# Kernel optimization log

Hardware: AMD Instinct MI355X
Metric: run time of the kernel (lower is better)

Reference implementation:

```python
import jax, jax.numpy as jnp
import numpy as np

D_MODEL = 192
D_STATE = 16
D_CONV = 4
EXPAND = 2
D_INNER = EXPAND * D_MODEL          # 384
DT_RANK = (D_MODEL + 15) // 16       # 12
B_, C_, DD, HH, WW = 2, 192, 32, 32, 16


def setup_inputs() -> dict:
    key = jax.random.key(0)
    ks = jax.random.split(key, 10)
    s = 0.02
    return {
        "x": jax.random.normal(ks[0], (B_, C_, DD, HH, WW), jnp.float32),
        # Mamba params (mamba-ssm layout)
        "in_proj_w": jax.random.normal(ks[1], (2 * D_INNER, D_MODEL), jnp.float32) * s,
        "conv_w": jax.random.normal(ks[2], (D_INNER, 1, D_CONV), jnp.float32) * s,
        "conv_b": jnp.zeros((D_INNER,), jnp.float32),
        "x_proj_w": jax.random.normal(ks[3], (DT_RANK + 2 * D_STATE, D_INNER), jnp.float32) * s,
        "dt_proj_w": jax.random.normal(ks[4], (D_INNER, DT_RANK), jnp.float32) * s,
        # bias chosen so softplus(dt) is small/positive, as in mamba's dt init
        "dt_proj_b": jax.random.uniform(ks[5], (D_INNER,), jnp.float32, minval=-4.0, maxval=-2.0),
        "A_log": jnp.log(jnp.broadcast_to(jnp.arange(1, D_STATE + 1, dtype=jnp.float32), (D_INNER, D_STATE))),
        "D_param": jnp.ones((D_INNER,), jnp.float32),
        "out_proj_w": jax.random.normal(ks[6], (D_MODEL, D_INNER), jnp.float32) * s,
        # 1x1x1 Conv3d projection (input_dim -> output_dim)
        "proj_w": jax.random.normal(ks[7], (C_, C_), jnp.float32) * s,
        "proj_b": jnp.zeros((C_,), jnp.float32),
    }


def _mamba(xf, in_proj_w, conv_w, conv_b, x_proj_w, dt_proj_w, dt_proj_b, A_log, D_param, out_proj_w):
    # xf: (B, L, d_model)
    B, L, _ = xf.shape
    xz = xf @ in_proj_w.T                          # (B, L, 2*d_inner)
    u, z = jnp.split(xz, 2, axis=-1)               # each (B, L, d_inner)

    # causal depthwise conv1d over L, kernel D_CONV
    uc = jnp.transpose(u, (0, 2, 1))               # (B, d_inner, L)
    up = jnp.pad(uc, ((0, 0), (0, 0), (D_CONV - 1, 0)))
    conv = sum(up[:, :, k:k + L] * conv_w[None, :, 0, k, None] for k in range(D_CONV))
    conv = conv + conv_b[None, :, None]
    u = jax.nn.silu(jnp.transpose(conv, (0, 2, 1)))  # (B, L, d_inner)

    dbl = u @ x_proj_w.T                           # (B, L, dt_rank + 2*d_state)
    dt_low = dbl[..., :DT_RANK]
    Bm = dbl[..., DT_RANK:DT_RANK + D_STATE]       # (B, L, d_state)
    Cm = dbl[..., DT_RANK + D_STATE:]              # (B, L, d_state)
    dt = jax.nn.softplus(dt_low @ dt_proj_w.T + dt_proj_b)  # (B, L, d_inner)

    A = -jnp.exp(A_log)                            # (d_inner, d_state)

    def step(h, inputs):
        u_t, dt_t, B_t, C_t = inputs               # (B,d_inner),(B,d_inner),(B,d_state),(B,d_state)
        dA = jnp.exp(dt_t[..., None] * A)          # (B, d_inner, d_state)
        h = dA * h + dt_t[..., None] * B_t[:, None, :] * u_t[..., None]
        y = jnp.einsum('bds,bs->bd', h, C_t)
        return h, y

    h0 = jnp.zeros((B, D_INNER, D_STATE), xf.dtype)
    xs = (jnp.transpose(u, (1, 0, 2)), jnp.transpose(dt, (1, 0, 2)),
          jnp.transpose(Bm, (1, 0, 2)), jnp.transpose(Cm, (1, 0, 2)))
    _, ys = jax.lax.scan(step, h0, xs)             # ys: (L, B, d_inner)
    y = jnp.transpose(ys, (1, 0, 2)) + u * D_param
    y = y * jax.nn.silu(z)
    return y @ out_proj_w.T                        # (B, L, d_model)


def reference(x, in_proj_w, conv_w, conv_b, x_proj_w, dt_proj_w, dt_proj_b,
              A_log, D_param, out_proj_w, proj_w, proj_b):
    B, C, Dz, H, W = x.shape
    # InstanceNorm3d (affine=False, eps=1e-5, biased variance)
    mu = x.mean(axis=(2, 3, 4), keepdims=True)
    var = x.var(axis=(2, 3, 4), keepdims=True)
    xn = (x - mu) / jnp.sqrt(var + 1e-5)
    L = Dz * H * W
    xf = jnp.transpose(xn.reshape(B, C, L), (0, 2, 1))  # (B, L, C)
    y = _mamba(xf, in_proj_w, conv_w, conv_b, x_proj_w, dt_proj_w, dt_proj_b,
               A_log, D_param, out_proj_w)
    y = jnp.transpose(y, (0, 2, 1)).reshape(B, C, Dz, H, W)
    # 1x1x1 Conv3d projection
    out = jnp.einsum('bcdhw,oc->bodhw', y, proj_w) + proj_b[None, :, None, None, None]
    return out
```

## Files before the change

kernel.cpp:

```cpp
#include <hip/hip_runtime.h>
#include <hip/hip_bf16.h>
#include <hip/hip_fp16.h>
#include <math.h>

#define BB   2
#define CM   192
#define DI   384
#define LL   16384
#define NST  16
#define RDT  12
#define XJ   44
#define NC   512
#define CLEN 32
#define NCH  (NC / 16)
#define DBS  64
#define XZS  768
#define CVT  32
#define BK   32

typedef __attribute__((ext_vector_type(8))) short bf16x8;
typedef __attribute__((ext_vector_type(4))) float f32x4;
typedef __attribute__((ext_vector_type(2))) float f32x2;
typedef unsigned short ushort_t;

static __device__ __forceinline__ ushort_t f2bf(float f) {
  __hip_bfloat16 h = __float2bfloat16(f);
  return *reinterpret_cast<ushort_t*>(&h);
}
static __device__ __forceinline__ float bf2f(ushort_t u) {
  __hip_bfloat16 h;
  *reinterpret_cast<ushort_t*>(&h) = u;
  return __bfloat162float(h);
}
static __device__ __forceinline__ ushort_t f2h(float f) {
  __half h = __float2half(f);
  return *reinterpret_cast<ushort_t*>(&h);
}
static __device__ __forceinline__ float h2f(ushort_t u) {
  __half h;
  *reinterpret_cast<ushort_t*>(&h) = u;
  return __half2float(h);
}
static __device__ __forceinline__ unsigned pk2bf(float lo, float hi) {
  return (unsigned)f2bf(lo) | ((unsigned)f2bf(hi) << 16);
}

__global__ __launch_bounds__(256) void fuse_proj_kernel(
    const float* __restrict__ pw, const float* __restrict__ ow, float* __restrict__ PW) {
  int idx = blockIdx.x * 256 + threadIdx.x;
  if (idx >= CM * DI) return;
  int o = idx / DI, d = idx % DI;
  float s = 0.f;
  #pragma unroll 4
  for (int c = 0; c < CM; c++) s += pw[o * CM + c] * ow[c * DI + d];
  PW[idx] = s;
}

__global__ __launch_bounds__(256) void cvt_weights_kernel(
    const float* __restrict__ ipw, const float* __restrict__ xpw,
    const float* __restrict__ PW,
    ushort_t* __restrict__ ipw_bf, ushort_t* __restrict__ xpw_bf,
    ushort_t* __restrict__ PW_bf) {
  int i = blockIdx.x * 256 + threadIdx.x;
  if (i < 2 * DI * CM) ipw_bf[i] = f2bf(ipw[i]);
  if (i < 128 * DI) {
    int r = i / DI;
    xpw_bf[i] = (r < XJ) ? f2bf(xpw[i]) : (ushort_t)0;
  }
  if (i < 256 * DI) {
    int r = i / DI;
    PW_bf[i] = (r < CM) ? f2bf(PW[i]) : (ushort_t)0;
  }
}

__global__ __launch_bounds__(256) void norm_stats_kernel(
    const float* __restrict__ x, float* __restrict__ mu, float* __restrict__ rstd) {
  int bc = blockIdx.x;
  const float* p = x + (size_t)bc * LL;
  float s = 0.f, ss = 0.f;
  for (int i = threadIdx.x * 4; i < LL; i += 256 * 4) {
    float4 v = *(const float4*)(p + i);
    s += v.x + v.y + v.z + v.w;
    ss += v.x * v.x + v.y * v.y + v.z * v.z + v.w * v.w;
  }
  for (int o = 32; o > 0; o >>= 1) {
    s += __shfl_down(s, o, 64);
    ss += __shfl_down(ss, o, 64);
  }
  __shared__ float sb[4], ssb[4];
  int wid = threadIdx.x >> 6;
  if ((threadIdx.x & 63) == 0) { sb[wid] = s; ssb[wid] = ss; }
  __syncthreads();
  if (threadIdx.x == 0) {
    s = sb[0] + sb[1] + sb[2] + sb[3];
    ss = ssb[0] + ssb[1] + ssb[2] + ssb[3];
    float m = s * (1.f / LL);
    float var = ss * (1.f / LL) - m * m;
    mu[bc] = m;
    rstd[bc] = 1.f / sqrtf(var + 1e-5f);
  }
}

__global__ __launch_bounds__(256) void xt_norm_kernel(
    const float* __restrict__ x, const float* __restrict__ mu,
    const float* __restrict__ rstd, ushort_t* __restrict__ xT) {
  __shared__ ushort_t T[64][72];
  int t0 = blockIdx.x * 64, c0 = blockIdx.y * 64, b = blockIdx.z;
  int tid = threadIdx.x;
  int c = tid >> 2, tq = (tid & 3) * 16;
  int bc = b * CM + c0 + c;
  const float* xp = x + (size_t)bc * LL + t0 + tq;
  float m = mu[bc], rs = rstd[bc];
  #pragma unroll
  for (int j = 0; j < 16; j += 4) {
    float4 v = *(const float4*)(xp + j);
    T[c][tq + j + 0] = f2bf((v.x - m) * rs);
    T[c][tq + j + 1] = f2bf((v.y - m) * rs);
    T[c][tq + j + 2] = f2bf((v.z - m) * rs);
    T[c][tq + j + 3] = f2bf((v.w - m) * rs);
  }
  __syncthreads();
  int t = tid >> 2, cq = (tid & 3) * 16;
  unsigned int ob[8];
  #pragma unroll
  for (int j = 0; j < 8; j++)
    ob[j] = (unsigned int)T[cq + 2 * j][t] | ((unsigned int)T[cq + 2 * j + 1][t] << 16);
  ushort_t* op = xT + ((size_t)b * LL + t0 + t) * CM + c0 + cq;
  *(uint4*)(op)     = make_uint4(ob[0], ob[1], ob[2], ob[3]);
  *(uint4*)(op + 8) = make_uint4(ob[4], ob[5], ob[6], ob[7]);
}

template <bool TOUT, typename OutT>
__global__ __launch_bounds__(256) void gemm_lds(
    const ushort_t* __restrict__ A, const ushort_t* __restrict__ BT,
    OutT* __restrict__ C, int K, int Mreal, int MT,
    long strideBT, long strideC, int ldc,
    const float* __restrict__ bias) {
  __shared__ ushort_t Asm[2][128 * BK];
  __shared__ ushort_t Bsm[2][128 * BK];

  int id = blockIdx.x;
  int per = MT * 8;
  int g = id / per, r = id % per;
  int nt = g * 8 + (r & 7);
  int mt = r >> 3;
  int b  = nt >> 7;
  long n0 = (long)(nt & 127) * 128;
  int m0 = mt * 128;

  int tid = threadIdx.x;
  int lane = tid & 63, wave = tid >> 6;
  const ushort_t* Bbase = BT + (size_t)b * strideBT;

  int srow0 = wave * 32 + (lane >> 2);
  int sk = (lane & 3) * 8;

  f32x4 acc[4][4];
  #pragma unroll
  for (int mi = 0; mi < 4; mi++)
    #pragma unroll
    for (int ni = 0; ni < 4; ni++) acc[mi][ni] = (f32x4){0.f, 0.f, 0.f, 0.f};

  int mh = wave & 1, nh = wave >> 1;
  int fr = lane & 15, fk = (lane >> 4) * 8;

  int nsteps = K / BK;
  {
    const ushort_t* As0 = A + (size_t)(m0 + srow0) * K + sk;
    const ushort_t* Bs0 = Bbase + (size_t)(n0 + srow0) * K + sk;
    __builtin_amdgcn_global_load_lds(As0, &Asm[0][wave * 1024], 16, 0, 0);
    __builtin_amdgcn_global_load_lds(As0 + (size_t)16 * K, &Asm[0][wave * 1024 + 512], 16, 0, 0);
    __builtin_amdgcn_global_load_lds(Bs0, &Bsm[0][wave * 1024], 16, 0, 0);
    __builtin_amdgcn_global_load_lds(Bs0 + (size_t)16 * K, &Bsm[0][wave * 1024 + 512], 16, 0, 0);
  }
  __syncthreads();
  int cur = 0;
  for (int s = 0; s < nsteps; s++) {
    if (s + 1 < nsteps) {
      int k0 = (s + 1) * BK;
      const ushort_t* As0 = A + (size_t)(m0 + srow0) * K + k0 + sk;
      const ushort_t* Bs0 = Bbase + (size_t)(n0 + srow0) * K + k0 + sk;
      __builtin_amdgcn_global_load_lds(As0, &Asm[cur ^ 1][wave * 1024], 16, 0, 0);
      __builtin_amdgcn_global_load_lds(As0 + (size_t)16 * K, &Asm[cur ^ 1][wave * 1024 + 512], 16, 0, 0);
      __builtin_amdgcn_global_load_lds(Bs0, &Bsm[cur ^ 1][wave * 1024], 16, 0, 0);
      __builtin_amdgcn_global_load_lds(Bs0 + (size_t)16 * K, &Bsm[cur ^ 1][wave * 1024 + 512], 16, 0, 0);
    }
    bf16x8 fa[4], fb[4];
    #pragma unroll
    for (int mi = 0; mi < 4; mi++)
      fa[mi] = *(const bf16x8*)&Asm[cur][(mh * 64 + mi * 16 + fr) * BK + fk];
    #pragma unroll
    for (int ni = 0; ni < 4; ni++)
      fb[ni] = *(const bf16x8*)&Bsm[cur][(nh * 64 + ni * 16 + fr) * BK + fk];
    #pragma unroll
    for (int mi = 0; mi < 4; mi++)
      #pragma unroll
      for (int ni = 0; ni < 4; ni++) {
        if constexpr (TOUT)
          acc[mi][ni] = __builtin_amdgcn_mfma_f32_16x16x32_bf16(fb[ni], fa[mi], acc[mi][ni], 0, 0, 0);
        else
          acc[mi][ni] = __builtin_amdgcn_mfma_f32_16x16x32_bf16(fa[mi], fb[ni], acc[mi][ni], 0, 0, 0);
      }
    __syncthreads();
    cur ^= 1;
  }

  int cq = (lane >> 4) * 4;
  if constexpr (TOUT) {
    #pragma unroll
    for (int ni = 0; ni < 4; ni++)
      #pragma unroll
      for (int rg = 0; rg < 4; rg++) {
        long n = n0 + nh * 64 + ni * 16 + cq + rg;
        OutT* cp = C + (size_t)b * strideC + n * ldc + m0 + mh * 64 + fr;
        #pragma unroll
        for (int mi = 0; mi < 4; mi++) {
          int mrow = m0 + mh * 64 + mi * 16 + fr;
          if (mrow < Mreal) {
            float v = acc[mi][ni][rg];
            if constexpr (sizeof(OutT) == 2) cp[mi * 16] = f2bf(v);
            else                             cp[mi * 16] = v;
          }
        }
      }
  } else {
    #pragma unroll
    for (int mi = 0; mi < 4; mi++)
      #pragma unroll
      for (int rg = 0; rg < 4; rg++) {
        int m = m0 + mh * 64 + mi * 16 + cq + rg;
        if (m < Mreal) {
          float bv = bias ? bias[m] : 0.f;
          OutT* cp = C + (size_t)b * strideC + (size_t)m * ldc + n0 + nh * 64 + fr;
          #pragma unroll
          for (int ni = 0; ni < 4; ni++)
            cp[ni * 16] = acc[mi][ni][rg] + bv;
        }
      }
  }
}

__global__ __launch_bounds__(384) void conv_silu_kernel(
    const ushort_t* __restrict__ xzT, const float* __restrict__ conv_w,
    const float* __restrict__ conv_b, ushort_t* __restrict__ u_t) {
  __shared__ ushort_t Us[CVT + 3][DI];
  int t0 = blockIdx.x * CVT;
  int b = blockIdx.y;
  int tid = threadIdx.x;
  #pragma unroll
  for (int r = 0; r < CVT + 3; r++) {
    int t = t0 - 3 + r;
    Us[r][tid] = (t >= 0) ? xzT[((size_t)b * LL + t) * XZS + tid] : (ushort_t)0;
  }
  float w0 = conv_w[tid * 4 + 0], w1 = conv_w[tid * 4 + 1];
  float w2 = conv_w[tid * 4 + 2], w3 = conv_w[tid * 4 + 3];
  float cb = conv_b[tid];
  __syncthreads();
  ushort_t* up = u_t + ((size_t)b * LL + t0) * DI + tid;
  float xm3 = bf2f(Us[0][tid]);
  float xm2 = bf2f(Us[1][tid]);
  float xm1 = bf2f(Us[2][tid]);
  #pragma unroll
  for (int t = 0; t < CVT; t++) {
    float xc = bf2f(Us[t + 3][tid]);
    float a = cb + w3 * xc + w2 * xm1 + w1 * xm2 + w0 * xm3;
    float sv = a / (1.f + __expf(-a));
    up[(size_t)t * DI] = f2bf(sv);
    xm3 = xm2; xm2 = xm1; xm1 = xc;
  }
}

__global__ __launch_bounds__(128) void scan_phase1(
    const ushort_t* __restrict__ u_t, const float* __restrict__ dblT,
    const float* __restrict__ A_log,
    const float* __restrict__ dtw, const float* __restrict__ dtb,
    ushort_t* __restrict__ hend, float* __restrict__ Sbuf,
    ushort_t* __restrict__ dt16) {
  int chunk = blockIdx.x, b = blockIdx.z;
  int d = blockIdx.y * 128 + threadIdx.x;
  int t0 = chunk * CLEN;
  const float* dblB = dblT + ((size_t)b * LL + t0) * DBS;
  int bd = b * DI + d;
  float av0 = -expf(A_log[d * NST]);
  float av_[NST];
  bool ok = true;
  #pragma unroll
  for (int j = 0; j < NST; j++) {
    av_[j] = -expf(A_log[d * NST + j]);
    ok = ok && (fabsf(av_[j] - av0 * (float)(j + 1)) <= 1e-4f * fabsf(av_[j]));
  }
  float w12[12];
  #pragma unroll
  for (int rr = 0; rr < 12; rr += 4)
    *(float4*)(w12 + rr) = *(const float4*)(dtw + d * 12 + rr);
  float db = dtb[d];
  const ushort_t* up = u_t + ((size_t)b * LL + t0) * DI + d;
  ushort_t* dtp16 = dt16 + ((size_t)b * LL + t0) * DI + d;
  float S = 0.f;

  size_t o = ((size_t)bd * NC + chunk) * NST;
  if (__all(ok)) {
    f32x2 h2[8];
    #pragma unroll
    for (int j = 0; j < 8; j++) h2[j] = (f32x2){0.f, 0.f};
    #pragma unroll 4
    for (int t = 0; t < CLEN; t++) {
      float4 L0 = *(const float4*)(dblB + t * DBS + 0);
      float4 L1 = *(const float4*)(dblB + t * DBS + 4);
      float4 L2 = *(const float4*)(dblB + t * DBS + 8);
      float4 B0 = *(const float4*)(dblB + t * DBS + RDT + 0);
      float4 B1 = *(const float4*)(dblB + t * DBS + RDT + 4);
      float4 B2 = *(const float4*)(dblB + t * DBS + RDT + 8);
      float4 B3 = *(const float4*)(dblB + t * DBS + RDT + 12);
      float acc = db;
      acc = fmaf(L0.x, w12[0], acc); acc = fmaf(L0.y, w12[1], acc);
      acc = fmaf(L0.z, w12[2], acc); acc = fmaf(L0.w, w12[3], acc);
      acc = fmaf(L1.x, w12[4], acc); acc = fmaf(L1.y, w12[5], acc);
      acc = fmaf(L1.z, w12[6], acc); acc = fmaf(L1.w, w12[7], acc);
      acc = fmaf(L2.x, w12[8], acc); acc = fmaf(L2.y, w12[9], acc);
      acc = fmaf(L2.z, w12[10], acc); acc = fmaf(L2.w, w12[11], acc);
      float dtv = (acc > 15.f) ? acc : __logf(1.f + __expf(acc));
      dtp16[(size_t)t * DI] = f2h(dtv);
      float uv  = bf2f(up[(size_t)t * DI]);
      float q = dtv * uv;
      S += dtv;
      float p1 = __expf(dtv * av0);
      float p2 = p1 * p1, p4 = p2 * p2, p8 = p4 * p4;
      f32x2 p2v = {p2, p2}, p4v = {p4, p4}, p8v = {p8, p8};
      f32x2 P0 = {p1, p2};
      f32x2 P1 = P0 * p2v;
      f32x2 P2 = P0 * p4v;
      f32x2 P3 = P1 * p4v;
      f32x2 P4 = P0 * p8v;
      f32x2 P5 = P1 * p8v;
      f32x2 P6 = P2 * p8v;
      f32x2 P7 = P3 * p8v;
      f32x2 qv = {q, q};
      h2[0] = P0 * h2[0] + qv * (f32x2){B0.x, B0.y};
      h2[1] = P1 * h2[1] + qv * (f32x2){B0.z, B0.w};
      h2[2] = P2 * h2[2] + qv * (f32x2){B1.x, B1.y};
      h2[3] = P3 * h2[3] + qv * (f32x2){B1.z, B1.w};
      h2[4] = P4 * h2[4] + qv * (f32x2){B2.x, B2.y};
      h2[5] = P5 * h2[5] + qv * (f32x2){B2.z, B2.w};
      h2[6] = P6 * h2[6] + qv * (f32x2){B3.x, B3.y};
      h2[7] = P7 * h2[7] + qv * (f32x2){B3.z, B3.w};
    }
    unsigned pk[8];
    #pragma unroll
    for (int j = 0; j < 8; j++) pk[j] = pk2bf(h2[j].x, h2[j].y);
    *(uint4*)(hend + o)     = make_uint4(pk[0], pk[1], pk[2], pk[3]);
    *(uint4*)(hend + o + 8) = make_uint4(pk[4], pk[5], pk[6], pk[7]);
  } else {
    float h[NST];
    #pragma unroll
    for (int j = 0; j < NST; j++) h[j] = 0.f;
    for (int t = 0; t < CLEN; t++) {
      float acc = db;
      #pragma unroll
      for (int rr = 0; rr < 12; rr++) acc = fmaf(dblB[t * DBS + rr], w12[rr], acc);
      float dtv = (acc > 15.f) ? acc : __logf(1.f + __expf(acc));
      dtp16[(size_t)t * DI] = f2h(dtv);
      float uv  = bf2f(up[(size_t)t * DI]);
      float q = dtv * uv;
      S += dtv;
      #pragma unroll
      for (int j = 0; j < NST; j++)
        h[j] = __expf(dtv * av_[j]) * h[j] + q * dblB[t * DBS + RDT + j];
    }
    #pragma unroll
    for (int j = 0; j < NST; j++) hend[o + j] = f2bf(h[j]);
  }
  Sbuf[(size_t)bd * NC + chunk] = S;
}

__global__ __launch_bounds__(256) void scan_combine(
    ushort_t* __restrict__ hend, const float* __restrict__ Sbuf,
    const float* __restrict__ A_log) {
  __shared__ float sP[16][16], sH[16][16];
  int bd = blockIdx.x;
  int d = bd % DI;
  int s = threadIdx.x & 15, g = threadIdx.x >> 4;
  float av = -expf(A_log[d * NST + s]);
  size_t baseS = (size_t)bd * NC + g * NCH;
  size_t base = ((size_t)bd * NC + g * NCH) * NST + s;
  float Pl = 1.f, Hl = 0.f;
  #pragma unroll
  for (int k = 0; k < NCH; k++) {
    float p = __expf(Sbuf[baseS + k] * av);
    Hl = fmaf(p, Hl, bf2f(hend[base + (size_t)k * NST]));
    Pl *= p;
  }
  sP[g][s] = Pl; sH[g][s] = Hl;
  __syncthreads();
  if (threadIdx.x < 16) {
    int ss = threadIdx.x;
    float c = 0.f;
    #pragma unroll
    for (int gg = 0; gg < 16; gg++) {
      float tmp = sH[gg][ss];
      float pp  = sP[gg][ss];
      sH[gg][ss] = c;
      c = fmaf(pp, c, tmp);
    }
  }
  __syncthreads();
  float c = sH[g][s];
  #pragma unroll
  for (int k = 0; k < NCH; k++) {
    size_t o = base + (size_t)k * NST;
    float p = __expf(Sbuf[baseS + k] * av);
    float he = bf2f(hend[o]);
    hend[o] = f2bf(c);
    c = fmaf(p, c, he);
  }
}

__global__ __launch_bounds__(128) void scan_phase3(
    const ushort_t* __restrict__ u_t, const float* __restrict__ dblT,
    const float* __restrict__ A_log, const ushort_t* __restrict__ dt16,
    const ushort_t* __restrict__ hin, const float* __restrict__ Dp,
    const ushort_t* __restrict__ xzT, ushort_t* __restrict__ ym_t) {
  int chunk = blockIdx.x, b = blockIdx.z;
  int d = blockIdx.y * 128 + threadIdx.x;
  int t0 = chunk * CLEN;
  const float* dblB = dblT + ((size_t)b * LL + t0) * DBS;
  int bd = b * DI + d;
  float av0 = -expf(A_log[d * NST]);
  float av_[NST];
  bool ok = true;
  #pragma unroll
  for (int j = 0; j < NST; j++) {
    av_[j] = -expf(A_log[d * NST + j]);
    ok = ok && (fabsf(av_[j] - av0 * (float)(j + 1)) <= 1e-4f * fabsf(av_[j]));
  }
  const ushort_t* up = u_t + ((size_t)b * LL + t0) * DI + d;
  const ushort_t* zp = xzT + ((size_t)b * LL + t0) * XZS + DI + d;
  const ushort_t* dtp16 = dt16 + ((size_t)b * LL + t0) * DI + d;
  ushort_t* ymp = ym_t + ((size_t)b * LL + t0) * DI + d;

  const ushort_t* hi = hin + ((size_t)bd * NC + chunk) * NST;
  float Dv = Dp[d];

  if (__all(ok)) {
    f32x2 h2[8];
    {
      uint4 q0 = *(const uint4*)(hi);
      uint4 q1 = *(const uint4*)(hi + 8);
      const unsigned* qw0 = (const unsigned*)&q0;
      const unsigned* qw1 = (const unsigned*)&q1;
      #pragma unroll
      for (int j = 0; j < 4; j++) {
        h2[j]     = (f32x2){bf2f((ushort_t)(qw0[j] & 0xffff)), bf2f((ushort_t)(qw0[j] >> 16))};
        h2[j + 4] = (f32x2){bf2f((ushort_t)(qw1[j] & 0xffff)), bf2f((ushort_t)(qw1[j] >> 16))};
      }
    }
    #pragma unroll 4
    for (int t = 0; t < CLEN; t++) {
      float4 B0 = *(const float4*)(dblB + t * DBS + RDT + 0);
      float4 B1 = *(const float4*)(dblB + t * DBS + RDT + 4);
      float4 B2 = *(const float4*)(dblB + t * DBS + RDT + 8);
      float4 B3 = *(const float4*)(dblB + t * DBS + RDT + 12);
      float4 C0 = *(const float4*)(dblB + t * DBS + RDT + 16);
      float4 C1 = *(const float4*)(dblB + t * DBS + RDT + 20);
      float4 C2 = *(const float4*)(dblB + t * DBS + RDT + 24);
      float4 C3 = *(const float4*)(dblB + t * DBS + RDT + 28);
      float dtv = h2f(dtp16[(size_t)t * DI]);
      float uv  = bf2f(up[(size_t)t * DI]);
      float zv  = bf2f(zp[(size_t)t * XZS]);
      float q = dtv * uv;
      float p1 = __expf(dtv * av0);
      float p2 = p1 * p1, p4 = p2 * p2, p8 = p4 * p4;
      f32x2 p2v = {p2, p2}, p4v = {p4, p4}, p8v = {p8, p8};
      f32x2 P0 = {p1, p2};
      f32x2 P1 = P0 * p2v;
      f32x2 P2 = P0 * p4v;
      f32x2 P3 = P1 * p4v;
      f32x2 P4 = P0 * p8v;
      f32x2 P5 = P1 * p8v;
      f32x2 P6 = P2 * p8v;
      f32x2 P7 = P3 * p8v;
      f32x2 qv = {q, q};
      f32x2 ya, yb;
      h2[0] = P0 * h2[0] + qv * (f32x2){B0.x, B0.y};  ya = h2[0] * (f32x2){C0.x, C0.y};
      h2[1] = P1 * h2[1] + qv * (f32x2){B0.z, B0.w};  yb = h2[1] * (f32x2){C0.z, C0.w};
      h2[2] = P2 * h2[2] + qv * (f32x2){B1.x, B1.y};  ya = h2[2] * (f32x2){C1.x, C1.y} + ya;
      h2[3] = P3 * h2[3] + qv * (f32x2){B1.z, B1.w};  yb = h2[3] * (f32x2){C1.z, C1.w} + yb;
      h2[4] = P4 * h2[4] + qv * (f32x2){B2.x, B2.y};  ya = h2[4] * (f32x2){C2.x, C2.y} + ya;
      h2[5] = P5 * h2[5] + qv * (f32x2){B2.z, B2.w};  yb = h2[5] * (f32x2){C2.z, C2.w} + yb;
      h2[6] = P6 * h2[6] + qv * (f32x2){B3.x, B3.y};  ya = h2[6] * (f32x2){C3.x, C3.y} + ya;
      h2[7] = P7 * h2[7] + qv * (f32x2){B3.z, B3.w};  yb = h2[7] * (f32x2){C3.z, C3.w} + yb;
      float y = (ya.x + ya.y) + (yb.x + yb.y);
      float yv = (y + uv * Dv) * (zv / (1.f + __expf(-zv)));
      ymp[(size_t)t * DI] = f2bf(yv);
    }
  } else {
    float h[NST];
    #pragma unroll
    for (int j = 0; j < NST; j++) h[j] = bf2f(hi[j]);
    for (int t = 0; t < CLEN; t++) {
      float dtv = h2f(dtp16[(size_t)t * DI]);
      float uv  = bf2f(up[(size_t)t * DI]);
      float zv  = bf2f(zp[(size_t)t * XZS]);
      float q = dtv * uv;
      float y = 0.f;
      #pragma unroll
      for (int j = 0; j < NST; j++) {
        h[j] = __expf(dtv * av_[j]) * h[j] + q * dblB[t * DBS + RDT + j];
        y = fmaf(h[j], dblB[t * DBS + RDT + NST + j], y);
      }
      float yv = (y + uv * Dv) * (zv / (1.f + __expf(-zv)));
      ymp[(size_t)t * DI] = f2bf(yv);
    }
  }
}

extern "C" void kernel_launch(void* const* d_in, const int* in_sizes, int n_in,
                              void* d_out, int out_size, void* d_ws, size_t ws_size,
                              hipStream_t stream) {
  const float* x         = (const float*)d_in[0];
  const float* in_proj_w = (const float*)d_in[1];
  const float* conv_w    = (const float*)d_in[2];
  const float* conv_b    = (const float*)d_in[3];
  const float* x_proj_w  = (const float*)d_in[4];
  const float* dt_proj_w = (const float*)d_in[5];
  const float* dt_proj_b = (const float*)d_in[6];
  const float* A_log     = (const float*)d_in[7];
  const float* D_param   = (const float*)d_in[8];
  const float* out_proj_w= (const float*)d_in[9];
  const float* proj_w    = (const float*)d_in[10];
  const float* proj_b    = (const float*)d_in[11];
  float* out = (float*)d_out;

  float* w = (float*)d_ws;
  float*    mu     = w;
  float*    rstd   = w + 512;
  float*    PW     = w + 1024;
  ushort_t* PW_bf  = (ushort_t*)(w + 74752);
  ushort_t* ipw_bf = (ushort_t*)(w + 123904);
  ushort_t* xpw_bf = (ushort_t*)(w + 197632);
  ushort_t* xT     = (ushort_t*)(w + 222208);
  ushort_t* xzT    = (ushort_t*)(w + 3367936);
  ushort_t* u_t    = (ushort_t*)(w + 15950848);
  float*    dblT   = w + 22242304;
  ushort_t* ym_t   = (ushort_t*)(w + 24339456);
  ushort_t* hend   = (ushort_t*)(w + 30630912);
  float*    Sbuf   = w + 33776640;
  ushort_t* dt16   = (ushort_t*)(w + 34169856);
  size_t need = 40461312;
  if (ws_size < need * sizeof(float)) return;

  norm_stats_kernel<<<dim3(BB * CM), dim3(256), 0, stream>>>(x, mu, rstd);
  fuse_proj_kernel<<<dim3((CM * DI + 255) / 256), dim3(256), 0, stream>>>(proj_w, out_proj_w, PW);
  cvt_weights_kernel<<<dim3((2 * DI * CM + 255) / 256), dim3(256), 0, stream>>>(
      in_proj_w, x_proj_w, PW, ipw_bf, xpw_bf, PW_bf);
  xt_norm_kernel<<<dim3(LL / 64, CM / 64, BB), dim3(256), 0, stream>>>(x, mu, rstd, xT);

  gemm_lds<true, ushort_t><<<dim3(256 * 6), dim3(256), 0, stream>>>(
      ipw_bf, xT, xzT, CM, 768, 6, (long)LL * CM, (long)LL * XZS, XZS, nullptr);

  conv_silu_kernel<<<dim3(LL / CVT, BB), dim3(384), 0, stream>>>(xzT, conv_w, conv_b, u_t);

  gemm_lds<true, float><<<dim3(256 * 1), dim3(256), 0, stream>>>(
      xpw_bf, u_t, dblT, DI, 64, 1, (long)LL * DI, (long)LL * DBS, DBS, nullptr);

  scan_phase1<<<dim3(NC, 3, BB), dim3(128), 0, stream>>>(
      u_t, dblT, A_log, dt_proj_w, dt_proj_b, hend, Sbuf, dt16);
  scan_combine<<<dim3(BB * DI), dim3(256), 0, stream>>>(hend, Sbuf, A_log);
  scan_phase3<<<dim3(NC, 3, BB), dim3(128), 0, stream>>>(
      u_t, dblT, A_log, dt16, hend, D_param, xzT, ym_t);

  gemm_lds<false, float><<<dim3(256 * 2), dim3(256), 0, stream>>>(
      PW_bf, ym_t, out, DI, CM, 2, (long)LL * DI, (long)CM * LL, LL, proj_b);
}
```

Measured before the change: 183.7 us.

## Compute intra-chunk scan output in phase1, add carried-state correction in phase3

Phase 1 of the chunked scan now also computes the zero-initial-state partial output y and the running cumulative dt within each chunk, storing both as 16-bit buffers. Phase 3 no longer re-runs the recurrence. It adds the carried-in state contribution, using the geometric structure of A to evaluate exp(Scum*A_j) cheaply. The silu of z moves into the in_proj GEMM epilogue. This trades the second full recurrence pass for one more buffer written and read, and adds precision risk from storing the cumulative dt sum in fp16.

Result: slower. 194.4 us (+5.8%).

```diff
diff --git a/kernel.cpp b/kernel.cpp
--- a/kernel.cpp
+++ b/kernel.cpp
@@ -130,7 +130,7 @@
   *(uint4*)(op + 8) = make_uint4(ob[4], ob[5], ob[6], ob[7]);
 }
 
-template <bool TOUT, typename OutT>
+template <bool TOUT, bool SILUZ, typename OutT>
 __global__ __launch_bounds__(256) void gemm_lds(
     const ushort_t* __restrict__ A, const ushort_t* __restrict__ BT,
     OutT* __restrict__ C, int K, int Mreal, int MT,
@@ -218,6 +218,9 @@
           int mrow = m0 + mh * 64 + mi * 16 + fr;
           if (mrow < Mreal) {
             float v = acc[mi][ni][rg];
+            if constexpr (SILUZ) {
+              if (mrow >= DI) v = v / (1.f + __expf(-v));
+            }
             if constexpr (sizeof(OutT) == 2) cp[mi * 16] = f2bf(v);
             else                             cp[mi * 16] = v;
           }
@@ -275,7 +278,7 @@
     const float* __restrict__ A_log,
     const float* __restrict__ dtw, const float* __restrict__ dtb,
     ushort_t* __restrict__ hend, float* __restrict__ Sbuf,
-    ushort_t* __restrict__ dt16) {
+    ushort_t* __restrict__ scum16, ushort_t* __restrict__ ypart) {
   int chunk = blockIdx.x, b = blockIdx.z;
   int d = blockIdx.y * 128 + threadIdx.x;
   int t0 = chunk * CLEN;
@@ -295,7 +298,8 @@
     *(float4*)(w12 + rr) = *(const float4*)(dtw + d * 12 + rr);
   float db = dtb[d];
   const ushort_t* up = u_t + ((size_t)b * LL + t0) * DI + d;
-  ushort_t* dtp16 = dt16 + ((size_t)b * LL + t0) * DI + d;
+  ushort_t* scp = scum16 + ((size_t)b * LL + t0) * DI + d;
+  ushort_t* ypp = ypart + ((size_t)b * LL + t0) * DI + d;
   float S = 0.f;
 
   size_t o = ((size_t)bd * NC + chunk) * NST;
@@ -312,6 +316,10 @@
       float4 B1 = *(const float4*)(dblB + t * DBS + RDT + 4);
       float4 B2 = *(const float4*)(dblB + t * DBS + RDT + 8);
       float4 B3 = *(const float4*)(dblB + t * DBS + RDT + 12);
+      float4 C0 = *(const float4*)(dblB + t * DBS + RDT + 16);
+      float4 C1 = *(const float4*)(dblB + t * DBS + RDT + 20);
+      float4 C2 = *(const float4*)(dblB + t * DBS + RDT + 24);
+      float4 C3 = *(const float4*)(dblB + t * DBS + RDT + 28);
       float acc = db;
       acc = fmaf(L0.x, w12[0], acc); acc = fmaf(L0.y, w12[1], acc);
       acc = fmaf(L0.z, w12[2], acc); acc = fmaf(L0.w, w12[3], acc);
@@ -320,154 +328,10 @@
       acc = fmaf(L2.x, w12[8], acc); acc = fmaf(L2.y, w12[9], acc);
       acc = fmaf(L2.z, w12[10], acc); acc = fmaf(L2.w, w12[11], acc);
       float dtv = (acc > 15.f) ? acc : __logf(1.f + __expf(acc));
-      dtp16[(size_t)t * DI] = f2h(dtv);
       float uv  = bf2f(up[(size_t)t * DI]);
       float q = dtv * uv;
       S += dtv;
-      float p1 = __expf(dtv * av0);
-      float p2 = p1 * p1, p4 = p2 * p2, p8 = p4 * p4;
-      f32x2 p2v = {p2, p2}, p4v = {p4, p4}, p8v = {p8, p8};
-      f32x2 P0 = {p1, p2};
-      f32x2 P1 = P0 * p2v;
-      f32x2 P2 = P0 * p4v;
-      f32x2 P3 = P1 * p4v;
-      f32x2 P4 = P0 * p8v;
-      f32x2 P5 = P1 * p8v;
-      f32x2 P6 = P2 * p8v;
-      f32x2 P7 = P3 * p8v;
-      f32x2 qv = {q, q};
-      h2[0] = P0 * h2[0] + qv * (f32x2){B0.x, B0.y};
-      h2[1] = P1 * h2[1] + qv * (f32x2){B0.z, B0.w};
-      h2[2] = P2 * h2[2] + qv * (f32x2){B1.x, B1.y};
-      h2[3] = P3 * h2[3] + qv * (f32x2){B1.z, B1.w};
-      h2[4] = P4 * h2[4] + qv * (f32x2){B2.x, B2.y};
-      h2[5] = P5 * h2[5] + qv * (f32x2){B2.z, B2.w};
-      h2[6] = P6 * h2[6] + qv * (f32x2){B3.x, B3.y};
-      h2[7] = P7 * h2[7] + qv * (f32x2){B3.z, B3.w};
-    }
-    unsigned pk[8];
-    #pragma unroll
-    for (int j = 0; j < 8; j++) pk[j] = pk2bf(h2[j].x, h2[j].y);
-    *(uint4*)(hend + o)     = make_uint4(pk[0], pk[1], pk[2], pk[3]);
-    *(uint4*)(hend + o + 8) = make_uint4(pk[4], pk[5], pk[6], pk[7]);
-  } else {
-    float h[NST];
-    #pragma unroll
-    for (int j = 0; j < NST; j++) h[j] = 0.f;
-    for (int t = 0; t < CLEN; t++) {
-      float acc = db;
-      #pragma unroll
-      for (int rr = 0; rr < 12; rr++) acc = fmaf(dblB[t * DBS + rr], w12[rr], acc);
-      float dtv = (acc > 15.f) ? acc : __logf(1.f + __expf(acc));
-      dtp16[(size_t)t * DI] = f2h(dtv);
-      float uv  = bf2f(up[(size_t)t * DI]);
-      float q = dtv * uv;
-      S += dtv;
-      #pragma unroll
-      for (int j = 0; j < NST; j++)
-        h[j] = __expf(dtv * av_[j]) * h[j] + q * dblB[t * DBS + RDT + j];
-    }
-    #pragma unroll
-    for (int j = 0; j < NST; j++) hend[o + j] = f2bf(h[j]);
-  }
-  Sbuf[(size_t)bd * NC + chunk] = S;
-}
-
-__global__ __launch_bounds__(256) void scan_combine(
-    ushort_t* __restrict__ hend, const float* __restrict__ Sbuf,
-    const float* __restrict__ A_log) {
-  __shared__ float sP[16][16], sH[16][16];
-  int bd = blockIdx.x;
-  int d = bd % DI;
-  int s = threadIdx.x & 15, g = threadIdx.x >> 4;
-  float av = -expf(A_log[d * NST + s]);
-  size_t baseS = (size_t)bd * NC + g * NCH;
-  size_t base = ((size_t)bd * NC + g * NCH) * NST + s;
-  float Pl = 1.f, Hl = 0.f;
-  #pragma unroll
-  for (int k = 0; k < NCH; k++) {
-    float p = __expf(Sbuf[baseS + k] * av);
-    Hl = fmaf(p, Hl, bf2f(hend[base + (size_t)k * NST]));
-    Pl *= p;
-  }
-  sP[g][s] = Pl; sH[g][s] = Hl;
-  __syncthreads();
-  if (threadIdx.x < 16) {
-    int ss = threadIdx.x;
-    float c = 0.f;
-    #pragma unroll
-    for (int gg = 0; gg < 16; gg++) {
-      float tmp = sH[gg][ss];
-      float pp  = sP[gg][ss];
-      sH[gg][ss] = c;
-      c = fmaf(pp, c, tmp);
-    }
-  }
-  __syncthreads();
-  float c = sH[g][s];
-  #pragma unroll
-  for (int k = 0; k < NCH; k++) {
-    size_t o = base + (size_t)k * NST;
-    float p = __expf(Sbuf[baseS + k] * av);
-    float he = bf2f(hend[o]);
-    hend[o] = f2bf(c);
-    c = fmaf(p, c, he);
-  }
-}
-
-__global__ __launch_bounds__(128) void scan_phase3(
-    const ushort_t* __restrict__ u_t, const float* __restrict__ dblT,
-    const float* __restrict__ A_log, const ushort_t* __restrict__ dt16,
-    const ushort_t* __restrict__ hin, const float* __restrict__ Dp,
-    const ushort_t* __restrict__ xzT, ushort_t* __restrict__ ym_t) {
-  int chunk = blockIdx.x, b = blockIdx.z;
-  int d = blockIdx.y * 128 + threadIdx.x;
-  int t0 = chunk * CLEN;
-  const float* dblB = dblT + ((size_t)b * LL + t0) * DBS;
-  int bd = b * DI + d;
-  float av0 = -expf(A_log[d * NST]);
-  float av_[NST];
-  bool ok = true;
-  #pragma unroll
-  for (int j = 0; j < NST; j++) {
-    av_[j] = -expf(A_log[d * NST + j]);
-    ok = ok && (fabsf(av_[j] - av0 * (float)(j + 1)) <= 1e-4f * fabsf(av_[j]));
-  }
-  const ushort_t* up = u_t + ((size_t)b * LL + t0) * DI + d;
-  const ushort_t* zp = xzT + ((size_t)b * LL + t0) * XZS + DI + d;
-  const ushort_t* dtp16 = dt16 + ((size_t)b * LL + t0) * DI + d;
-  ushort_t* ymp = ym_t + ((size_t)b * LL + t0) * DI + d;
-
-  const ushort_t* hi = hin + ((size_t)bd * NC + chunk) * NST;
-  float Dv = Dp[d];
-
-  if (__all(ok)) {
-    f32x2 h2[8];
-    {
-      uint4 q0 = *(const uint4*)(hi);
-      uint4 q1 = *(const uint4*)(hi + 8);
-      const unsigned* qw0 = (const unsigned*)&q0;
-      const unsigned* qw1 = (const unsigned*)&q1;
-      #pragma unroll
-      for (int j = 0; j < 4; j++) {
-        h2[j]     = (f32x2){bf2f((ushort_t)(qw0[j] & 0xffff)), bf2f((ushort_t)(qw0[j] >> 16))};
-        h2[j + 4] = (f32x2){bf2f((ushort_t)(qw1[j] & 0xffff)), bf2f((ushort_t)(qw1[j] >> 16))};
-      }
-    }
-    #pragma unroll 4
-    for (int t = 0; t < CLEN; t++) {
-      float4 B0 = *(const float4*)(dblB + t * DBS + RDT + 0);
-      float4 B1 = *(const float4*)(dblB + t * DBS + RDT + 4);
-      float4 B2 = *(const float4*)(dblB + t * DBS + RDT + 8);
-      float4 B3 = *(const float4*)(dblB + t * DBS + RDT + 12);
-      float4 C0 = *(const float4*)(dblB + t * DBS + RDT + 16);
-      float4 C1 = *(const float4*)(dblB + t * DBS + RDT + 20);
-      float4 C2 = *(const float4*)(dblB + t * DBS + RDT + 24);
-      float4 C3 = *(const float4*)(dblB + t * DBS + RDT + 28);
-      float dtv = h2f(dtp16[(size_t)t * DI]);
-      float uv  = bf2f(up[(size_t)t * DI]);
-      float zv  = bf2f(zp[(size_t)t * XZS]);
-      float q = dtv * uv;
+      scp[(size_t)t * DI] = f2h(S);
       float p1 = __expf(dtv * av0);
       float p2 = p1 * p1, p4 = p2 * p2, p8 = p4 * p4;
       f32x2 p2v = {p2, p2}, p4v = {p4, p4}, p8v = {p8, p8};
@@ -489,26 +353,173 @@
       h2[5] = P5 * h2[5] + qv * (f32x2){B2.z, B2.w};  yb = h2[5] * (f32x2){C2.z, C2.w} + yb;
       h2[6] = P6 * h2[6] + qv * (f32x2){B3.x, B3.y};  ya = h2[6] * (f32x2){C3.x, C3.y} + ya;
       h2[7] = P7 * h2[7] + qv * (f32x2){B3.z, B3.w};  yb = h2[7] * (f32x2){C3.z, C3.w} + yb;
-      float y = (ya.x + ya.y) + (yb.x + yb.y);
-      float yv = (y + uv * Dv) * (zv / (1.f + __expf(-zv)));
-      ymp[(size_t)t * DI] = f2bf(yv);
-    }
+      float yp = (ya.x + ya.y) + (yb.x + yb.y);
+      ypp[(size_t)t * DI] = f2bf(yp);
+    }
+    unsigned pk[8];
+    #pragma unroll
+    for (int j = 0; j < 8; j++) pk[j] = pk2bf(h2[j].x, h2[j].y);
+    *(uint4*)(hend + o)     = make_uint4(pk[0], pk[1], pk[2], pk[3]);
+    *(uint4*)(hend + o + 8) = make_uint4(pk[4], pk[5], pk[6], pk[7]);
   } else {
     float h[NST];
     #pragma unroll
-    for (int j = 0; j < NST; j++) h[j] = bf2f(hi[j]);
+    for (int j = 0; j < NST; j++) h[j] = 0.f;
     for (int t = 0; t < CLEN; t++) {
-      float dtv = h2f(dtp16[(size_t)t * DI]);
+      float acc = db;
+      #pragma unroll
+      for (int rr = 0; rr < 12; rr++) acc = fmaf(dblB[t * DBS + rr], w12[rr], acc);
+      float dtv = (acc > 15.f) ? acc : __logf(1.f + __expf(acc));
       float uv  = bf2f(up[(size_t)t * DI]);
-      float zv  = bf2f(zp[(size_t)t * XZS]);
       float q = dtv * uv;
-      float y = 0.f;
+      S += dtv;
+      scp[(size_t)t * DI] = f2h(S);
+      float yp = 0.f;
       #pragma unroll
       for (int j = 0; j < NST; j++) {
         h[j] = __expf(dtv * av_[j]) * h[j] + q * dblB[t * DBS + RDT + j];
-        y = fmaf(h[j], dblB[t * DBS + RDT + NST + j], y);
+        yp = fmaf(h[j], dblB[t * DBS + RDT + NST + j], yp);
       }
-      float yv = (y + uv * Dv) * (zv / (1.f + __expf(-zv)));
+      ypp[(size_t)t * DI] = f2bf(yp);
+    }
+    #pragma unroll
+    for (int j = 0; j < NST; j++) hend[o + j] = f2bf(h[j]);
+  }
+  Sbuf[(size_t)bd * NC + chunk] = S;
+}
+
+__global__ __launch_bounds__(256) void scan_combine(
+    ushort_t* __restrict__ hend, const float* __restrict__ Sbuf,
+    const float* __restrict__ A_log) {
+  __shared__ float sP[16][16], sH[16][16];
+  int bd = blockIdx.x;
+  int d = bd % DI;
+  int s = threadIdx.x & 15, g = threadIdx.x >> 4;
+  float av = -expf(A_log[d * NST + s]);
+  size_t baseS = (size_t)bd * NC + g * NCH;
+  size_t base = ((size_t)bd * NC + g * NCH) * NST + s;
+  float Pl = 1.f, Hl = 0.f;
+  #pragma unroll
+  for (int k = 0; k < NCH; k++) {
+    float p = __expf(Sbuf[baseS + k] * av);
+    Hl = fmaf(p, Hl, bf2f(hend[base + (size_t)k * NST]));
+    Pl *= p;
+  }
+  sP[g][s] = Pl; sH[g][s] = Hl;
+  __syncthreads();
+  if (threadIdx.x < 16) {
+    int ss = threadIdx.x;
+    float c = 0.f;
+    #pragma unroll
+    for (int gg = 0; gg < 16; gg++) {
+      float tmp = sH[gg][ss];
+      float pp  = sP[gg][ss];
+      sH[gg][ss] = c;
+      c = fmaf(pp, c, tmp);
+    }
+  }
+  __syncthreads();
+  float c = sH[g][s];
+  #pragma unroll
+  for (int k = 0; k < NCH; k++) {
+    size_t o = base + (size_t)k * NST;
+    float p = __expf(Sbuf[baseS + k] * av);
+    float he = bf2f(hend[o]);
+    hend[o] = f2bf(c);
+    c = fmaf(p, c, he);
+  }
+}
+
+__global__ __launch_bounds__(128) void scan_phase3(
+    const ushort_t* __restrict__ u_t, const float* __restrict__ dblT,
+    const float* __restrict__ A_log, const ushort_t* __restrict__ scum16,
+    const ushort_t* __restrict__ ypart, const ushort_t* __restrict__ hin,
+    const float* __restrict__ Dp,
+    const ushort_t* __restrict__ xzT, ushort_t* __restrict__ ym_t) {
+  int chunk = blockIdx.x, b = blockIdx.z;
+  int d = blockIdx.y * 128 + threadIdx.x;
+  int t0 = chunk * CLEN;
+  const float* dblB = dblT + ((size_t)b * LL + t0) * DBS;
+  int bd = b * DI + d;
+  float av0 = -expf(A_log[d * NST]);
+  float av_[NST];
+  bool ok = true;
+  #pragma unroll
+  for (int j = 0; j < NST; j++) {
+    av_[j] = -expf(A_log[d * NST + j]);
+    ok = ok && (fabsf(av_[j] - av0 * (float)(j + 1)) <= 1e-4f * fabsf(av_[j]));
+  }
+  const ushort_t* up = u_t + ((size_t)b * LL + t0) * DI + d;
+  const ushort_t* zp = xzT + ((size_t)b * LL + t0) * XZS + DI + d;
+  const ushort_t* scp = scum16 + ((size_t)b * LL + t0) * DI + d;
+  const ushort_t* ypp = ypart + ((size_t)b * LL + t0) * DI + d;
+  ushort_t* ymp = ym_t + ((size_t)b * LL + t0) * DI + d;
+
+  const ushort_t* hi = hin + ((size_t)bd * NC + chunk) * NST;
+  float Dv = Dp[d];
+
+  if (__all(ok)) {
+    f32x2 g[8];
+    {
+      uint4 q0 = *(const uint4*)(hi);
+      uint4 q1 = *(const uint4*)(hi + 8);
+      const unsigned* qw0 = (const unsigned*)&q0;
+      const unsigned* qw1 = (const unsigned*)&q1;
+      #pragma unroll
+      for (int j = 0; j < 4; j++) {
+        g[j]     = (f32x2){bf2f((ushort_t)(qw0[j] & 0xffff)), bf2f((ushort_t)(qw0[j] >> 16))};
+        g[j + 4] = (f32x2){bf2f((ushort_t)(qw1[j] & 0xffff)), bf2f((ushort_t)(qw1[j] >> 16))};
+      }
+    }
+    #pragma unroll 4
+    for (int t = 0; t < CLEN; t++) {
+      float4 C0 = *(const float4*)(dblB + t * DBS + RDT + 16);
+      float4 C1 = *(const float4*)(dblB + t * DBS + RDT + 20);
+      float4 C2 = *(const float4*)(dblB + t * DBS + RDT + 24);
+      float4 C3 = *(const float4*)(dblB + t * DBS + RDT + 28);
+      float Scum = h2f(scp[(size_t)t * DI]);
+      float uv = bf2f(up[(size_t)t * DI]);
+      float zs = bf2f(zp[(size_t)t * XZS]);
+      float yp = bf2f(ypp[(size_t)t * DI]);
+      float w1 = __expf(Scum * av0);
+      float w2s = w1 * w1;
+      f32x2 w2v = {w2s, w2s};
+      f32x2 cg0 = (f32x2){C0.x, C0.y} * g[0];
+      f32x2 cg1 = (f32x2){C0.z, C0.w} * g[1];
+      f32x2 cg2 = (f32x2){C1.x, C1.y} * g[2];
+      f32x2 cg3 = (f32x2){C1.z, C1.w} * g[3];
+      f32x2 cg4 = (f32x2){C2.x, C2.y} * g[4];
+      f32x2 cg5 = (f32x2){C2.z, C2.w} * g[5];
+      f32x2 cg6 = (f32x2){C3.x, C3.y} * g[6];
+      f32x2 cg7 = (f32x2){C3.z, C3.w} * g[7];
+      f32x2 acc = cg7;
+      acc = cg6 + w2v * acc;
+      acc = cg5 + w2v * acc;
+      acc = cg4 + w2v * acc;
+      acc = cg3 + w2v * acc;
+      acc = cg2 + w2v * acc;
+      acc = cg1 + w2v * acc;
+      acc = cg0 + w2v * acc;
+      float y2 = acc.x * w1 + acc.y * w2s;
+      float y = yp + y2;
+      float yv = (y + uv * Dv) * zs;
+      ymp[(size_t)t * DI] = f2bf(yv);
+    }
+  } else {
+    float gg[NST];
+    #pragma unroll
+    for (int j = 0; j < NST; j++) gg[j] = bf2f(hi[j]);
+    for (int t = 0; t < CLEN; t++) {
+      float Scum = h2f(scp[(size_t)t * DI]);
+      float uv = bf2f(up[(size_t)t * DI]);
+      float zs = bf2f(zp[(size_t)t * XZS]);
+      float y = bf2f(ypp[(size_t)t * DI]);
+      #pragma unroll
+      for (int j = 0; j < NST; j++) {
+        float wj = __expf(Scum * av_[j]);
+        y = fmaf(dblB[t * DBS + RDT + NST + j] * wj, gg[j], y);
+      }
+      float yv = (y + uv * Dv) * zs;
       ymp[(size_t)t * DI] = f2bf(yv);
     }
   }
@@ -545,8 +556,9 @@
   ushort_t* ym_t   = (ushort_t*)(w + 24339456);
   ushort_t* hend   = (ushort_t*)(w + 30630912);
   float*    Sbuf   = w + 33776640;
-  ushort_t* dt16   = (ushort_t*)(w + 34169856);
-  size_t need = 40461312;
+  ushort_t* scum16 = (ushort_t*)(w + 34169856);
+  ushort_t* ypart  = (ushort_t*)(w + 40461312);
+  size_t need = 46752768;
   if (ws_size < need * sizeof(float)) return;
 
   norm_stats_kernel<<<dim3(BB * CM), dim3(256), 0, stream>>>(x, mu, rstd);
@@ -555,20 +567,20 @@
       in_proj_w, x_proj_w, PW, ipw_bf, xpw_bf, PW_bf);
   xt_norm_kernel<<<dim3(LL / 64, CM / 64, BB), dim3(256), 0, stream>>>(x, mu, rstd, xT);
 
-  gemm_lds<true, ushort_t><<<dim3(256 * 6), dim3(256), 0, stream>>>(
+  gemm_lds<true, true, ushort_t><<<dim3(256 * 6), dim3(256), 0, stream>>>(
       ipw_bf, xT, xzT, CM, 768, 6, (long)LL * CM, (long)LL * XZS, XZS, nullptr);
 
   conv_silu_kernel<<<dim3(LL / CVT, BB), dim3(384), 0, stream>>>(xzT, conv_w, conv_b, u_t);
 
-  gemm_lds<true, float><<<dim3(256 * 1), dim3(256), 0, stream>>>(
+  gemm_lds<true, false, float><<<dim3(256 * 1), dim3(256), 0, stream>>>(
       xpw_bf, u_t, dblT, DI, 64, 1, (long)LL * DI, (long)LL * DBS, DBS, nullptr);
 
   scan_phase1<<<dim3(NC, 3, BB), dim3(128), 0, stream>>>(
-      u_t, dblT, A_log, dt_proj_w, dt_proj_b, hend, Sbuf, dt16);
+      u_t, dblT, A_log, dt_proj_w, dt_proj_b, hend, Sbuf, scum16, ypart);
   scan_combine<<<dim3(BB * DI), dim3(256), 0, stream>>>(hend, Sbuf, A_log);
   scan_phase3<<<dim3(NC, 3, BB), dim3(128), 0, stream>>>(
-      u_t, dblT, A_log, dt16, hend, D_param, xzT, ym_t);
-
-  gemm_lds<false, float><<<dim3(256 * 2), dim3(256), 0, stream>>>(
+      u_t, dblT, A_log, scum16, ypart, hend, D_param, xzT, ym_t);
+
+  gemm_lds<false, false, float><<<dim3(256 * 2), dim3(256), 0, stream>>>(
       PW_bf, ym_t, out, DI, CM, 2, (long)LL * DI, (long)CM * LL, LL, proj_b);
 }
```
